# Performance work log

Measured on AMD Instinct MI355X. Metric: run time of the kernel, lower is better.

## Reference

```python
import jax, jax.numpy as jnp
import numpy as np

B, XD, PD, D, H = 512, 32768, 512, 64, 128  # batch, x_dim, proj_dim, latent_dim, per_dim_hidden
G1 = 1024  # gene projector hidden (hardcoded in module)


def _init(k, shape, fan_in):
    s = 1.0 / np.sqrt(fan_in)
    return jax.random.uniform(k, shape, jnp.float32, -s, s)


def setup_inputs() -> dict:
    key = jax.random.key(0)
    ks = jax.random.split(key, 16)
    return {
        "x": jax.random.normal(ks[0], (B, XD), jnp.float32),
        "z": jax.random.normal(ks[1], (B, D), jnp.float32),
        "perm": jax.random.permutation(ks[2], B).astype(jnp.int32),
        # shared gene projector
        "Wg1": _init(ks[3], (XD, G1), XD), "bg1": _init(ks[4], (G1,), XD),
        "Wg2": _init(ks[5], (G1, PD), G1), "bg2": _init(ks[6], (PD,), G1),
        # per-dimension 3-layer MLPs, stacked over D. Layer-1 weight [PD+1, H]
        # is split into the h-part Wh and the z-part Wz (last input column).
        "Wh": _init(ks[7], (D, PD, H), PD + 1),
        "Wz": _init(ks[8], (D, H), PD + 1),
        "b1": _init(ks[9], (D, H), PD + 1),
        "W2": _init(ks[10], (D, H, H), H), "b2": _init(ks[11], (D, H), H),
        "W3": _init(ks[12], (D, H), H), "b3": _init(ks[13], (D,), H),
    }


def reference(x, z, perm, Wg1, bg1, Wg2, bg2, Wh, Wz, b1, W2, b2, W3, b3):
    elu = jax.nn.elu
    # shared gene projector (eval mode: dropout = identity, no noise)
    h = elu(elu(x @ Wg1 + bg1) @ Wg2 + bg2)            # [B, PD]
    # batched layer-1 of all D per-dim nets; h-projection computed once and
    # reused for the marginal pass via permutation (h_shuffled = h[perm]).
    hWh = jnp.einsum('bp,dph->bdh', h, Wh)             # [B, D, H]
    zWz = z[:, :, None] * Wz[None]                     # [B, D, H]

    def head(a1_pre):
        a1 = elu(a1_pre)                               # [B, D, H]
        a2 = elu(jnp.einsum('bdh,dhk->bdk', a1, W2) + b2)
        return jnp.einsum('bdh,dh->bd', a2, W3) + b3   # [B, D] scalar scores

    joint_score = head(hWh + zWz + b1)                 # T(h, z_j)
    marg_score = head(hWh[perm] + zWz + b1)            # T(h_shuffled, z_j)

    emas = jnp.ones((D,), x.dtype)                     # buffer init = ones, eval: no update
    et = jnp.mean(jnp.exp(marg_score), axis=0)         # [D]
    mi = jnp.mean(joint_score, axis=0) - jnp.log(et / emas)
    return -jnp.mean(mi)
```

## Files before the change

### kernel.cpp

```cpp
#include <hip/hip_runtime.h>
#include <hip/hip_bf16.h>
#include <math.h>

#define B_  512
#define XD_ 32768
#define PD_ 512
#define D_  64
#define H_  128
#define G1_ 1024

typedef __attribute__((ext_vector_type(8))) short short8v;
typedef __attribute__((ext_vector_type(4))) float floatx4;

__device__ __forceinline__ float eluf(float v) { return v > 0.f ? v : expm1f(v); }

__device__ __forceinline__ void split8t(const float* c, short8v& h, short8v& l) {
    unsigned hu[8], lu[8];
    #pragma unroll
    for (int j = 0; j < 8; j++) {
        unsigned u = __float_as_uint(c[j]);
        hu[j] = u & 0xFFFF0000u;
        float res = c[j] - __uint_as_float(hu[j]);
        lu[j] = __float_as_uint(res);
    }
    uint4 hp, lp;
    hp.x = __builtin_amdgcn_perm(hu[1], hu[0], 0x07060302u);
    hp.y = __builtin_amdgcn_perm(hu[3], hu[2], 0x07060302u);
    hp.z = __builtin_amdgcn_perm(hu[5], hu[4], 0x07060302u);
    hp.w = __builtin_amdgcn_perm(hu[7], hu[6], 0x07060302u);
    lp.x = __builtin_amdgcn_perm(lu[1], lu[0], 0x07060302u);
    lp.y = __builtin_amdgcn_perm(lu[3], lu[2], 0x07060302u);
    lp.z = __builtin_amdgcn_perm(lu[5], lu[4], 0x07060302u);
    lp.w = __builtin_amdgcn_perm(lu[7], lu[6], 0x07060302u);
    h = __builtin_bit_cast(short8v, hp);
    l = __builtin_bit_cast(short8v, lp);
}

__global__ __launch_bounds__(256) void k_trs(const float* __restrict__ x,
                                             ushort* __restrict__ xh,
                                             ushort* __restrict__ xl) {
    const int k0 = blockIdx.x * 64;
    const int m0 = blockIdx.y * 64;
    const int t = threadIdx.x;
    const int m = t & 63;
    const int kq = t >> 6;
    #pragma unroll
    for (int i = 0; i < 2; i++) {
        int kg = kq * 2 + i;
        const float* p = x + (size_t)(m0 + m) * XD_ + k0 + kg * 8;
        float4 v0 = *(const float4*)p, v1 = *(const float4*)(p + 4);
        float c[8] = {v0.x, v0.y, v0.z, v0.w, v1.x, v1.y, v1.z, v1.w};
        short8v h, l; split8t(c, h, l);
        size_t off = ((size_t)((k0 >> 3) + kg) * B_ + m0 + m) * 8;
        *(short8v*)(xh + off) = h;
        *(short8v*)(xl + off) = l;
    }
}

__global__ __launch_bounds__(256, 2) void k_gemm1t(const ushort* __restrict__ xh,
                                                   const ushort* __restrict__ xl,
                                                   const float* __restrict__ Wg1,
                                                   float* __restrict__ part,
                                                   int KS) {
    __shared__ ushort Ah[2][4 * 128 * 8], Al[2][4 * 128 * 8];
    __shared__ ushort Bh[2][4 * 128 * 8], Bl[2][4 * 128 * 8];
    const int nt = blockIdx.x, mt = blockIdx.y, ks = blockIdx.z;
    const int t = threadIdx.x;
    const int w = t >> 6, lane = t & 63;
    const int q = lane >> 4, l15 = lane & 15;
    const int wr = w >> 1, wc = w & 1;
    const int q4 = t >> 6, pr = t & 63;
    const int k0 = ks * KS;

    const size_t aoff = (((size_t)(k0 >> 3) + q4) * B_ + mt * 128 + pr) * 8;
    const ushort* Agh = xh + aoff;
    const ushort* Agl = xl + aoff;
    const float*  Bg  = Wg1 + (size_t)(k0 + q4 * 8) * G1_ + nt * 128 + pr * 2;

    floatx4 acc[4][4];
    #pragma unroll
    for (int i = 0; i < 4; i++)
        #pragma unroll
        for (int j = 0; j < 4; j++) acc[i][j] = (floatx4){0.f, 0.f, 0.f, 0.f};

    uint4 pAh0, pAh1, pAl0, pAl1;
    float2 pb[8];

    auto loadT = [&](int kt) {
        size_t o = (size_t)kt * B_;
        pAh0 = *(const uint4*)(Agh + o);
        pAh1 = *(const uint4*)(Agh + o + 512);
        pAl0 = *(const uint4*)(Agl + o);
        pAl1 = *(const uint4*)(Agl + o + 512);
        const float* p = Bg + (size_t)kt * G1_;
        #pragma unroll
        for (int kk = 0; kk < 8; kk++) pb[kk] = *(const float2*)(p + (size_t)kk * G1_);
    };

    auto stage = [&](int buf) {
        float c0[8], c1[8];
        #pragma unroll
        for (int kk = 0; kk < 8; kk++) { c0[kk] = pb[kk].x; c1[kk] = pb[kk].y; }
        short8v bh0, bl0, bh1, bl1;
        split8t(c0, bh0, bl0); split8t(c1, bh1, bl1);
        int n0 = pr * 2;
        int i0 = (q4 * 128 + (n0 ^ q4)) * 8;
        int i1 = (q4 * 128 + ((n0 + 1) ^ q4)) * 8;
        *(short8v*)&Bh[buf][i0] = bh0; *(short8v*)&Bl[buf][i0] = bl0;
        *(short8v*)&Bh[buf][i1] = bh1; *(short8v*)&Bl[buf][i1] = bl1;
        int ia0 = (q4 * 128 + (pr ^ q4)) * 8;
        *(uint4*)&Ah[buf][ia0] = pAh0;
        *(uint4*)&Al[buf][ia0] = pAl0;
        *(uint4*)&Ah[buf][ia0 + 512] = pAh1;
        *(uint4*)&Al[buf][ia0 + 512] = pAl1;
    };

    auto mma = [&](int buf) {
        short8v af[4], alf[4], bf[4], blf[4];
        #pragma unroll
        for (int i = 0; i < 4; i++) {
            int m = wr * 64 + i * 16 + l15;
            int idx = (q * 128 + (m ^ q)) * 8;
            af[i]  = *(const short8v*)&Ah[buf][idx];
            alf[i] = *(const short8v*)&Al[buf][idx];
        }
        #pragma unroll
        for (int j = 0; j < 4; j++) {
            int n = wc * 64 + j * 16 + l15;
            int idx = (q * 128 + (n ^ q)) * 8;
            bf[j]  = *(const short8v*)&Bh[buf][idx];
            blf[j] = *(const short8v*)&Bl[buf][idx];
        }
        #pragma unroll
        for (int i = 0; i < 4; i++)
            #pragma unroll
            for (int j = 0; j < 4; j++) {
                acc[i][j] = __builtin_amdgcn_mfma_f32_16x16x32_bf16(af[i],  bf[j],  acc[i][j], 0, 0, 0);
                acc[i][j] = __builtin_amdgcn_mfma_f32_16x16x32_bf16(af[i],  blf[j], acc[i][j], 0, 0, 0);
                acc[i][j] = __builtin_amdgcn_mfma_f32_16x16x32_bf16(alf[i], bf[j],  acc[i][j], 0, 0, 0);
            }
    };

    loadT(0);
    stage(0);
    loadT(32);
    asm volatile("s_waitcnt lgkmcnt(0)" ::: "memory");
    __builtin_amdgcn_s_barrier();

    const int NT = KS >> 5;
    for (int it = 0; it < NT - 1; it++) {
        const int cur = it & 1;
        stage(cur ^ 1);
        if (it + 2 < NT) loadT((it + 2) * 32);
        mma(cur);
        asm volatile("s_waitcnt lgkmcnt(0)" ::: "memory");
        __builtin_amdgcn_s_barrier();
    }
    mma((NT - 1) & 1);

    float* P = part + (size_t)ks * (B_ * G1_) + (size_t)(mt * 128) * G1_ + nt * 128;
    #pragma unroll
    for (int i = 0; i < 4; i++)
        #pragma unroll
        for (int j = 0; j < 4; j++) {
            int col = wc * 64 + j * 16 + l15;
            #pragma unroll
            for (int r = 0; r < 4; r++) {
                int row = wr * 64 + i * 16 + q * 4 + r;
                P[(size_t)row * G1_ + col] = acc[i][j][r];
            }
        }
}

__global__ __launch_bounds__(256, 2) void k_gemm1m(const float* __restrict__ x,
                                                   const float* __restrict__ Wg1,
                                                   float* __restrict__ part,
                                                   int KS) {
    __shared__ ushort Ah[4 * 128 * 8], Al[4 * 128 * 8];
    __shared__ ushort Bh[4 * 128 * 8], Bl[4 * 128 * 8];
    const int nt = blockIdx.x, mt = blockIdx.y, ks = blockIdx.z;
    const int t = threadIdx.x;
    const int w = t >> 6, lane = t & 63;
    const int q = lane >> 4, l15 = lane & 15;
    const int wr = w >> 1, wc = w & 1;
    const int kbB = t >> 6, nb = t & 63;
    const int mA = t & 127, kbA = t >> 7;
    const int k0 = ks * KS;

    const float* Ag = x + (size_t)(mt * 128 + mA) * XD_ + k0 + kbA * 8;
    const float* Bg = Wg1 + (size_t)(k0 + kbB * 8) * G1_ + nt * 128 + nb * 2;

    floatx4 acc[4][4];
    #pragma unroll
    for (int i = 0; i < 4; i++)
        #pragma unroll
        for (int j = 0; j < 4; j++) acc[i][j] = (floatx4){0.f, 0.f, 0.f, 0.f};

    float4 pa0 = *(const float4*)(Ag);
    float4 pa1 = *(const float4*)(Ag + 4);
    float4 pa2 = *(const float4*)(Ag + 16);
    float4 pa3 = *(const float4*)(Ag + 20);
    float2 pb[8];
    #pragma unroll
    for (int kk = 0; kk < 8; kk++) pb[kk] = *(const float2*)(Bg + (size_t)kk * G1_);

    for (int kt = 0; kt < KS; kt += 32) {
        float cA0[8] = {pa0.x, pa0.y, pa0.z, pa0.w, pa1.x, pa1.y, pa1.z, pa1.w};
        float cA1[8] = {pa2.x, pa2.y, pa2.z, pa2.w, pa3.x, pa3.y, pa3.z, pa3.w};
        float c0[8], c1[8];
        #pragma unroll
        for (int kk = 0; kk < 8; kk++) { c0[kk] = pb[kk].x; c1[kk] = pb[kk].y; }
        short8v ah0, al0, ah1, al1, bh0, bl0, bh1, bl1;
        split8t(cA0, ah0, al0);
        split8t(cA1, ah1, al1);
        split8t(c0, bh0, bl0);
        split8t(c1, bh1, bl1);
        if (kt + 32 < KS) {
            pa0 = *(const float4*)(Ag + kt + 32);
            pa1 = *(const float4*)(Ag + kt + 36);
            pa2 = *(const float4*)(Ag + kt + 48);
            pa3 = *(const float4*)(Ag + kt + 52);
            const float* p = Bg + (size_t)(kt + 32) * G1_;
            #pragma unroll
            for (int kk = 0; kk < 8; kk++) pb[kk] = *(const float2*)(p + (size_t)kk * G1_);
        }
        {
            int ia0 = (kbA * 128 + (mA ^ kbA)) * 8;
            int ia1 = ((kbA + 2) * 128 + (mA ^ (kbA + 2))) * 8;
            *(short8v*)&Ah[ia0] = ah0; *(short8v*)&Al[ia0] = al0;
            *(short8v*)&Ah[ia1] = ah1; *(short8v*)&Al[ia1] = al1;
            int n0i = nb * 2;
            int i0 = (kbB * 128 + (n0i ^ kbB)) * 8;
            int i1 = (kbB * 128 + ((n0i + 1) ^ kbB)) * 8;
            *(short8v*)&Bh[i0] = bh0; *(short8v*)&Bl[i0] = bl0;
            *(short8v*)&Bh[i1] = bh1; *(short8v*)&Bl[i1] = bl1;
        }
        __syncthreads();
        short8v af[4], alf[4], bf[4], blf[4];
        #pragma unroll
        for (int i = 0; i < 4; i++) {
            int m = wr * 64 + i * 16 + l15;
            int idx = (q * 128 + (m ^ q)) * 8;
            af[i]  = *(const short8v*)&Ah[idx];
            alf[i] = *(const short8v*)&Al[idx];
        }
        #pragma unroll
        for (int j = 0; j < 4; j++) {
            int n = wc * 64 + j * 16 + l15;
            int idx = (q * 128 + (n ^ q)) * 8;
            bf[j]  = *(const short8v*)&Bh[idx];
            blf[j] = *(const short8v*)&Bl[idx];
        }
        #pragma unroll
        for (int i = 0; i < 4; i++)
            #pragma unroll
            for (int j = 0; j < 4; j++) {
                acc[i][j] = __builtin_amdgcn_mfma_f32_16x16x32_bf16(af[i],  bf[j],  acc[i][j], 0, 0, 0);
                acc[i][j] = __builtin_amdgcn_mfma_f32_16x16x32_bf16(af[i],  blf[j], acc[i][j], 0, 0, 0);
                acc[i][j] = __builtin_amdgcn_mfma_f32_16x16x32_bf16(alf[i], bf[j],  acc[i][j], 0, 0, 0);
            }
        __syncthreads();
    }
    float* P = part + (size_t)ks * (B_ * G1_) + (size_t)(mt * 128) * G1_ + nt * 128;
    #pragma unroll
    for (int i = 0; i < 4; i++)
        #pragma unroll
        for (int j = 0; j < 4; j++) {
            int col = wc * 64 + j * 16 + l15;
            #pragma unroll
            for (int r = 0; r < 4; r++) {
                int row = wr * 64 + i * 16 + q * 4 + r;
                P[(size_t)row * G1_ + col] = acc[i][j][r];
            }
        }
}

__global__ __launch_bounds__(256) void k_red1(const float* __restrict__ part,
                                              const float* __restrict__ bg1,
                                              ushort* __restrict__ Gh,
                                              ushort* __restrict__ Gl,
                                              int nparts) {
    int idx = (blockIdx.x * 256 + threadIdx.x) * 8;
    const int S = B_ * G1_;
    float c[8] = {};
    for (int k = 0; k < nparts; k++) {
        const float* p = part + (size_t)k * S + idx;
        float4 v0 = *(const float4*)p, v1 = *(const float4*)(p + 4);
        c[0] += v0.x; c[1] += v0.y; c[2] += v0.z; c[3] += v0.w;
        c[4] += v1.x; c[5] += v1.y; c[6] += v1.z; c[7] += v1.w;
    }
    int cb = idx & (G1_ - 1);
    float4 b0 = *(const float4*)(bg1 + cb), b1v = *(const float4*)(bg1 + cb + 4);
    c[0] = eluf(c[0] + b0.x); c[1] = eluf(c[1] + b0.y);
    c[2] = eluf(c[2] + b0.z); c[3] = eluf(c[3] + b0.w);
    c[4] = eluf(c[4] + b1v.x); c[5] = eluf(c[5] + b1v.y);
    c[6] = eluf(c[6] + b1v.z); c[7] = eluf(c[7] + b1v.w);
    short8v h, l; split8t(c, h, l);
    *(short8v*)(Gh + idx) = h;
    *(short8v*)(Gl + idx) = l;
}

__global__ __launch_bounds__(256, 2) void k_gemm2m(const ushort* __restrict__ Gh,
                                                   const ushort* __restrict__ Gl,
                                                   const float* __restrict__ Wg2,
                                                   float* __restrict__ part2) {
    __shared__ ushort Ah[4 * 64 * 8], Al[4 * 64 * 8];
    __shared__ ushort Bh[4 * 64 * 8], Bl[4 * 64 * 8];
    const int nt = blockIdx.x, mt = blockIdx.y, ks = blockIdx.z;
    const int t = threadIdx.x;
    const int w = t >> 6, lane = t & 63;
    const int q = lane >> 4, l15 = lane & 15;
    const int kb = (t >> 4) & 3;
    const int rb = (t & 15) | (w << 4);
    const int k0 = ks * 128;

    const int cB = t & 63, g = t >> 6;

    floatx4 acc[4];
    #pragma unroll
    for (int i = 0; i < 4; i++) acc[i] = (floatx4){0.f, 0.f, 0.f, 0.f};

    for (int kt = 0; kt < 128; kt += 32) {
        {
            const ushort* pH = Gh + (size_t)(mt * 64 + rb) * G1_ + k0 + kt + kb * 8;
            const ushort* pL = Gl + (size_t)(mt * 64 + rb) * G1_ + k0 + kt + kb * 8;
            uint4 vh = *(const uint4*)pH;
            uint4 vl = *(const uint4*)pL;
            int idx = (kb * 64 + (rb ^ kb)) * 8;
            *(uint4*)&Ah[idx] = vh;
            *(uint4*)&Al[idx] = vl;
        }
        {
            float c[8];
            const float* p = Wg2 + (size_t)(k0 + kt + g * 8) * PD_ + nt * 64 + cB;
            #pragma unroll
            for (int kk = 0; kk < 8; kk++) c[kk] = p[(size_t)kk * PD_];
            short8v h, l; split8t(c, h, l);
            int idx = (g * 64 + (cB ^ g)) * 8;
            *(short8v*)&Bh[idx] = h;
            *(short8v*)&Bl[idx] = l;
        }
        __syncthreads();
        short8v af[4], alf[4], bf, blf;
        #pragma unroll
        for (int i = 0; i < 4; i++) {
            int m = i * 16 + l15;
            int idx = (q * 64 + (m ^ q)) * 8;
            af[i]  = *(const short8v*)&Ah[idx];
            alf[i] = *(const short8v*)&Al[idx];
        }
        {
            int n = w * 16 + l15;
            int idx = (q * 64 + (n ^ q)) * 8;
            bf  = *(const short8v*)&Bh[idx];
            blf = *(const short8v*)&Bl[idx];
        }
        #pragma unroll
        for (int i = 0; i < 4; i++) {
            acc[i] = __builtin_amdgcn_mfma_f32_16x16x32_bf16(af[i],  bf,  acc[i], 0, 0, 0);
            acc[i] = __builtin_amdgcn_mfma_f32_16x16x32_bf16(af[i],  blf, acc[i], 0, 0, 0);
            acc[i] = __builtin_amdgcn_mfma_f32_16x16x32_bf16(alf[i], bf,  acc[i], 0, 0, 0);
        }
        __syncthreads();
    }
    float* P = part2 + (size_t)ks * (B_ * PD_) + (size_t)(mt * 64) * PD_ + nt * 64;
    #pragma unroll
    for (int i = 0; i < 4; i++) {
        int col = w * 16 + l15;
        #pragma unroll
        for (int r = 0; r < 4; r++) {
            int row = i * 16 + q * 4 + r;
            P[(size_t)row * PD_ + col] = acc[i][r];
        }
    }
}

__global__ __launch_bounds__(256) void k_red2(const float* __restrict__ part2,
                                              const float* __restrict__ bg2,
                                              ushort* __restrict__ hh,
                                              ushort* __restrict__ hl) {
    int idx = (blockIdx.x * 256 + threadIdx.x) * 8;
    const int S = B_ * PD_;
    float c[8] = {};
    #pragma unroll
    for (int k = 0; k < 8; k++) {
        const float* p = part2 + (size_t)k * S + idx;
        float4 v0 = *(const float4*)p, v1 = *(const float4*)(p + 4);
        c[0] += v0.x; c[1] += v0.y; c[2] += v0.z; c[3] += v0.w;
        c[4] += v1.x; c[5] += v1.y; c[6] += v1.z; c[7] += v1.w;
    }
    int cb = idx & (PD_ - 1);
    float4 b0 = *(const float4*)(bg2 + cb), b1v = *(const float4*)(bg2 + cb + 4);
    c[0] = eluf(c[0] + b0.x); c[1] = eluf(c[1] + b0.y);
    c[2] = eluf(c[2] + b0.z); c[3] = eluf(c[3] + b0.w);
    c[4] = eluf(c[4] + b1v.x); c[5] = eluf(c[5] + b1v.y);
    c[6] = eluf(c[6] + b1v.z); c[7] = eluf(c[7] + b1v.w);
    short8v h, l; split8t(c, h, l);
    *(short8v*)(hh + idx) = h;
    *(short8v*)(hl + idx) = l;
}

__global__ __launch_bounds__(256, 2) void k_hwh_m(const ushort* __restrict__ hh,
                                                  const ushort* __restrict__ hl,
                                                  const float* __restrict__ Wh,
                                                  float* __restrict__ hWh) {
    __shared__ ushort Ah[4 * 64 * 8], Al[4 * 64 * 8];
    __shared__ ushort Bh[4 * 128 * 8], Bl[4 * 128 * 8];
    const int d = blockIdx.x, mt = blockIdx.y;
    const int t = threadIdx.x;
    const int w = t >> 6, lane = t & 63;
    const int q = lane >> 4, l15 = lane & 15;
    const int kb = (t >> 4) & 3;
    const int rb = (t & 15) | (w << 4);

    const ushort* AgH = hh + (size_t)(mt * 64 + rb) * PD_ + kb * 8;
    const ushort* AgL = hl + (size_t)(mt * 64 + rb) * PD_ + kb * 8;
    const float* Bg = Wh + (size_t)d * (PD_ * H_) + (size_t)(kb * 8) * H_ + rb * 2;

    floatx4 acc[4][2];
    #pragma unroll
    for (int i = 0; i < 4; i++)
        #pragma unroll
        for (int j = 0; j < 2; j++) acc[i][j] = (floatx4){0.f, 0.f, 0.f, 0.f};

    uint4 pah = *(const uint4*)(AgH);
    uint4 pal = *(const uint4*)(AgL);
    float2 pb[8];
    #pragma unroll
    for (int kk = 0; kk < 8; kk++) pb[kk] = *(const float2*)(Bg + (size_t)kk * H_);

    for (int kt = 0; kt < PD_; kt += 32) {
        float c0[8], c1[8];
        #pragma unroll
        for (int kk = 0; kk < 8; kk++) { c0[kk] = pb[kk].x; c1[kk] = pb[kk].y; }
        short8v bh0, bl0, bh1, bl1;
        split8t(c0, bh0, bl0);
        split8t(c1, bh1, bl1);
        uint4 ah = pah, al = pal;
        if (kt + 32 < PD_) {
            pah = *(const uint4*)(AgH + kt + 32);
            pal = *(const uint4*)(AgL + kt + 32);
            const float* p = Bg + (size_t)(kt + 32) * H_;
            #pragma unroll
            for (int kk = 0; kk < 8; kk++) pb[kk] = *(const float2*)(p + (size_t)kk * H_);
        }
        {
            int idx = (kb * 64 + (rb ^ kb)) * 8;
            *(uint4*)&Ah[idx] = ah;
            *(uint4*)&Al[idx] = al;
            int n0i = rb * 2;
            int i0 = (kb * 128 + (n0i ^ kb)) * 8;
            int i1 = (kb * 128 + ((n0i + 1) ^ kb)) * 8;
            *(short8v*)&Bh[i0] = bh0; *(short8v*)&Bl[i0] = bl0;
            *(short8v*)&Bh[i1] = bh1; *(short8v*)&Bl[i1] = bl1;
        }
        __syncthreads();
        short8v af[4], alf[4], bf[2], blf[2];
        #pragma unroll
        for (int i = 0; i < 4; i++) {
            int m = i * 16 + l15;
            int idx = (q * 64 + (m ^ q)) * 8;
            af[i]  = *(const short8v*)&Ah[idx];
            alf[i] = *(const short8v*)&Al[idx];
        }
        #pragma unroll
        for (int j = 0; j < 2; j++) {
            int n = w * 32 + j * 16 + l15;
            int idx = (q * 128 + (n ^ q)) * 8;
            bf[j]  = *(const short8v*)&Bh[idx];
            blf[j] = *(const short8v*)&Bl[idx];
        }
        #pragma unroll
        for (int i = 0; i < 4; i++)
            #pragma unroll
            for (int j = 0; j < 2; j++) {
                acc[i][j] = __builtin_amdgcn_mfma_f32_16x16x32_bf16(af[i],  bf[j],  acc[i][j], 0, 0, 0);
                acc[i][j] = __builtin_amdgcn_mfma_f32_16x16x32_bf16(af[i],  blf[j], acc[i][j], 0, 0, 0);
                acc[i][j] = __builtin_amdgcn_mfma_f32_16x16x32_bf16(alf[i], bf[j],  acc[i][j], 0, 0, 0);
            }
        __syncthreads();
    }
    #pragma unroll
    for (int i = 0; i < 4; i++)
        #pragma unroll
        for (int j = 0; j < 2; j++) {
            int col = w * 32 + j * 16 + l15;
            #pragma unroll
            for (int r = 0; r < 4; r++) {
                int row = i * 16 + q * 4 + r;
                int b = mt * 64 + row;
                hWh[(size_t)b * (D_ * H_) + d * H_ + col] = acc[i][j][r];
            }
        }
}

__global__ __launch_bounds__(256, 2) void k_heads(const float* __restrict__ hWh,
                                                  const float* __restrict__ z,
                                                  const int* __restrict__ perm,
                                                  const float* __restrict__ Wz,
                                                  const float* __restrict__ b1,
                                                  const float* __restrict__ W2,
                                                  const float* __restrict__ b2,
                                                  const float* __restrict__ W3,
                                                  const float* __restrict__ b3,
                                                  float* __restrict__ jpart,
                                                  float* __restrict__ epart) {
    const int chunk = blockIdx.x;
    const int d = blockIdx.y;
    const int pass = blockIdx.z;
    const int t = threadIdx.x;
    const int b0 = chunk * 64;
    __shared__ ushort A1h[16 * 64 * 8];
    __shared__ ushort A1l[16 * 64 * 8];
    __shared__ float  BS[4096];
    ushort* Bh = (ushort*)BS;
    ushort* Bl = Bh + 4096;
    float*  sred = BS;

    const int w = t >> 6, lane = t & 63;
    const int q = lane >> 4, l15 = lane & 15;
    const int kb = (t >> 4) & 3;
    const int rb = (t & 15) | (w << 4);

    const float* W2d = W2 + (size_t)d * H_ * H_;
    const float* Wzd = Wz + d * H_;
    const float* b1d = b1 + d * H_;
    const float* b2d = b2 + d * H_;
    const float* W3d = W3 + d * H_;

    {
        int i = t >> 2;
        int kt = t & 3;
        int h0 = kt * 32;
        int bb = b0 + i;
        int src = (pass == 0) ? bb : perm[bb];
        float zv = z[bb * D_ + d];
        const float* hrow = hWh + (size_t)src * (D_ * H_) + d * H_;
        #pragma unroll
        for (int kq = 0; kq < 4; kq++) {
            float c[8];
            int kbase = h0 + kq * 8;
            float4 v0 = *(const float4*)(hrow + kbase);
            float4 v1 = *(const float4*)(hrow + kbase + 4);
            float4 w0 = *(const float4*)(Wzd + kbase);
            float4 w1 = *(const float4*)(Wzd + kbase + 4);
            float4 x0 = *(const float4*)(b1d + kbase);
            float4 x1 = *(const float4*)(b1d + kbase + 4);
            c[0] = eluf(v0.x + zv * w0.x + x0.x);
            c[1] = eluf(v0.y + zv * w0.y + x0.y);
            c[2] = eluf(v0.z + zv * w0.z + x0.z);
            c[3] = eluf(v0.w + zv * w0.w + x0.w);
            c[4] = eluf(v1.x + zv * w1.x + x1.x);
            c[5] = eluf(v1.y + zv * w1.y + x1.y);
            c[6] = eluf(v1.z + zv * w1.z + x1.z);
            c[7] = eluf(v1.w + zv * w1.w + x1.w);
            short8v hv, lv; split8t(c, hv, lv);
            int idx = ((kt * 4 + kq) * 64 + (i ^ kq)) * 8;
            *(short8v*)&A1h[idx] = hv;
            *(short8v*)&A1l[idx] = lv;
        }
    }
    __syncthreads();
    floatx4 acc[4][2];
    #pragma unroll
    for (int i = 0; i < 4; i++)
        #pragma unroll
        for (int j = 0; j < 2; j++) acc[i][j] = (floatx4){0.f, 0.f, 0.f, 0.f};
    for (int kt2 = 0; kt2 < 4; kt2++) {
        {
            float c0[8], c1[8];
            const float* p = W2d + (size_t)(kt2 * 32 + kb * 8) * H_ + rb * 2;
            #pragma unroll
            for (int kk = 0; kk < 8; kk++) {
                float2 v = *(const float2*)(p + (size_t)kk * H_);
                c0[kk] = v.x; c1[kk] = v.y;
            }
            short8v h0v, l0v, h1v, l1v;
            split8t(c0, h0v, l0v);
            split8t(c1, h1v, l1v);
            int n0i = rb * 2;
            int i0 = (kb * 128 + (n0i ^ kb)) * 8;
            int i1 = (kb * 128 + ((n0i + 1) ^ kb)) * 8;
            *(short8v*)&Bh[i0] = h0v; *(short8v*)&Bl[i0] = l0v;
            *(short8v*)&Bh[i1] = h1v; *(short8v*)&Bl[i1] = l1v;
        }
        __syncthreads();
        short8v af[4], alf[4], bf[2], blf[2];
        #pragma unroll
        for (int i = 0; i < 4; i++) {
            int m = i * 16 + l15;
            int idx = ((kt2 * 4 + q) * 64 + (m ^ q)) * 8;
            af[i]  = *(const short8v*)&A1h[idx];
            alf[i] = *(const short8v*)&A1l[idx];
        }
        #pragma unroll
        for (int j = 0; j < 2; j++) {
            int n = w * 32 + j * 16 + l15;
            int idx = (q * 128 + (n ^ q)) * 8;
            bf[j]  = *(const short8v*)&Bh[idx];
            blf[j] = *(const short8v*)&Bl[idx];
        }
        #pragma unroll
        for (int i = 0; i < 4; i++)
            #pragma unroll
            for (int j = 0; j < 2; j++) {
                acc[i][j] = __builtin_amdgcn_mfma_f32_16x16x32_bf16(af[i],  bf[j],  acc[i][j], 0, 0, 0);
                acc[i][j] = __builtin_amdgcn_mfma_f32_16x16x32_bf16(af[i],  blf[j], acc[i][j], 0, 0, 0);
                acc[i][j] = __builtin_amdgcn_mfma_f32_16x16x32_bf16(alf[i], bf[j],  acc[i][j], 0, 0, 0);
            }
        __syncthreads();
    }
    #pragma unroll
    for (int i = 0; i < 4; i++) {
        #pragma unroll
        for (int r = 0; r < 4; r++) {
            int b = i * 16 + q * 4 + r;
            float s = 0.f;
            #pragma unroll
            for (int j = 0; j < 2; j++) {
                int col = w * 32 + j * 16 + l15;
                float a2v = eluf(acc[i][j][r] + b2d[col]);
                s = fmaf(a2v, W3d[col], s);
            }
            sred[b * 64 + w * 16 + l15] = s;
        }
    }
    __syncthreads();
    float val = 0.f;
    if (t < 64) {
        float s = b3[d];
        const float4* row = (const float4*)&sred[t * 64];
        #pragma unroll
        for (int c = 0; c < 16; c++) {
            float4 v = row[c];
            s += v.x + v.y + v.z + v.w;
        }
        val = (pass == 0) ? s : expf(s);
        #pragma unroll
        for (int off = 32; off > 0; off >>= 1)
            val += __shfl_down(val, off, 64);
    }
    if (t == 0) {
        if (pass == 0) jpart[d * 8 + chunk] = val;
        else           epart[d * 8 + chunk] = val;
    }
}

__global__ void k_final(const float* __restrict__ jpart,
                        const float* __restrict__ epart,
                        float* __restrict__ out) {
    int t = threadIdx.x;
    float mj = 0.f, me = 0.f;
    #pragma unroll
    for (int c = 0; c < 8; c++) { mj += jpart[t * 8 + c]; me += epart[t * 8 + c]; }
    mj *= (1.f / 512.f);
    me *= (1.f / 512.f);
    float mi = mj - logf(me);
    #pragma unroll
    for (int off = 32; off > 0; off >>= 1) mi += __shfl_down(mi, off, 64);
    if (t == 0) out[0] = -mi * (1.f / 64.f);
}

extern "C" void kernel_launch(void* const* d_in, const int* in_sizes, int n_in,
                              void* d_out, int out_size, void* d_ws, size_t ws_size,
                              hipStream_t stream) {
    const float* x   = (const float*)d_in[0];
    const float* z   = (const float*)d_in[1];
    const int*  perm = (const int*)d_in[2];
    const float* Wg1 = (const float*)d_in[3];
    const float* bg1 = (const float*)d_in[4];
    const float* Wg2 = (const float*)d_in[5];
    const float* bg2 = (const float*)d_in[6];
    const float* Wh  = (const float*)d_in[7];
    const float* Wz  = (const float*)d_in[8];
    const float* b1  = (const float*)d_in[9];
    const float* W2  = (const float*)d_in[10];
    const float* b2  = (const float*)d_in[11];
    const float* W3  = (const float*)d_in[12];
    const float* b3  = (const float*)d_in[13];
    float* out = (float*)d_out;

    char* base = (char*)d_ws;
    const size_t PART_SLICE = (size_t)B_ * G1_ * sizeof(float);

    const size_t NEW_NEED = 16 * PART_SLICE + 67108864ull + 2097152 + 1048576 + 4096;

    if (ws_size >= NEW_NEED) {
        float* part  = (float*)base;
        ushort* xh   = (ushort*)(base + 33554432);
        ushort* xl   = (ushort*)(base + 67108864);
        float* hWh   = (float*)base;
        float* part2 = (float*)(base + 16777216);
        ushort* Gh   = (ushort*)(base + 100663296);
        ushort* Gl   = Gh + 524288;
        ushort* hh   = (ushort*)(base + 102760448);
        ushort* hl   = hh + 262144;
        float* jpart = (float*)(base + 103809024);
        float* epart = jpart + 512;

        k_trs<<<dim3(512, 8), 256, 0, stream>>>(x, xh, xl);
        k_gemm1t<<<dim3(8, 4, 16), 256, 0, stream>>>(xh, xl, Wg1, part, XD_ / 16);
        k_red1<<<256, 256, 0, stream>>>(part, bg1, Gh, Gl, 16);
        k_gemm2m<<<dim3(8, 8, 8), 256, 0, stream>>>(Gh, Gl, Wg2, part2);
        k_red2<<<128, 256, 0, stream>>>(part2, bg2, hh, hl);
        k_hwh_m<<<dim3(64, 8), 256, 0, stream>>>(hh, hl, Wh, hWh);
        k_heads<<<dim3(8, 64, 2), 256, 0, stream>>>(hWh, z, perm, Wz, b1, W2, b2, W3, b3,
                                                    jpart, epart);
        k_final<<<1, 64, 0, stream>>>(jpart, epart, out);
    } else {
        int nks = (ws_size >= (size_t)32 * PART_SLICE + 3145728 + 4096) ? 32 : 16;
        const int KS = XD_ / nks;
        const size_t partBytes = (size_t)nks * PART_SLICE;

        float* part  = (float*)base;
        float* hWh   = (float*)base;
        float* part2 = (float*)(base + 16777216);
        ushort* Gh   = (ushort*)(base + partBytes);
        ushort* Gl   = Gh + 524288;
        ushort* hh   = (ushort*)(base + partBytes + 2097152);
        ushort* hl   = hh + 262144;
        float* jpart = (float*)(base + partBytes + 3145728);
        float* epart = jpart + 512;

        k_gemm1m<<<dim3(8, 4, nks), 256, 0, stream>>>(x, Wg1, part, KS);
        k_red1<<<256, 256, 0, stream>>>(part, bg1, Gh, Gl, nks);
        k_gemm2m<<<dim3(8, 8, 8), 256, 0, stream>>>(Gh, Gl, Wg2, part2);
        k_red2<<<128, 256, 0, stream>>>(part2, bg2, hh, hl);
        k_hwh_m<<<dim3(64, 8), 256, 0, stream>>>(hh, hl, Wh, hWh);
        k_heads<<<dim3(8, 64, 2), 256, 0, stream>>>(hWh, z, perm, Wz, b1, W2, b2, W3, b3,
                                                    jpart, epart);
        k_final<<<1, 64, 0, stream>>>(jpart, epart, out);
    }
}
```

Before: 427.8 us.

## Double-buffer hWh GEMM and merge joint/marginal head passes into one block

The per-dimension hWh GEMM now uses double-buffered LDS tiles and a load/stage/mma pipeline, so the next tile's global loads and bf16 splitting overlap the current MFMAs, with one barrier per step. The heads kernel runs both passes (joint and permuted) inside one block instead of a z-dimension of the grid. This halves the block count and lets the W2 loads hit cache on the second pass. The final row reduction is spread across all 256 threads via a small shared array. The costs are doubled LDS in the GEMM and less parallelism in the heads kernel.

Result: no change. 422.6 us (-1.2%).

```diff
diff --git a/kernel.cpp b/kernel.cpp
--- a/kernel.cpp
+++ b/kernel.cpp
@@ -108,11 +108,11 @@
         int i1 = (q4 * 128 + ((n0 + 1) ^ q4)) * 8;
         *(short8v*)&Bh[buf][i0] = bh0; *(short8v*)&Bl[buf][i0] = bl0;
         *(short8v*)&Bh[buf][i1] = bh1; *(short8v*)&Bl[buf][i1] = bl1;
-        int ia0 = (q4 * 128 + (pr ^ q4)) * 8;
-        *(uint4*)&Ah[buf][ia0] = pAh0;
-        *(uint4*)&Al[buf][ia0] = pAl0;
-        *(uint4*)&Ah[buf][ia0 + 512] = pAh1;
-        *(uint4*)&Al[buf][ia0 + 512] = pAl1;
+        int ia = (q4 * 128 + (pr ^ q4)) * 8;
+        *(uint4*)&Ah[buf][ia] = pAh0;
+        *(uint4*)&Al[buf][ia] = pAl0;
+        *(uint4*)&Ah[buf][ia + 512] = pAh1;
+        *(uint4*)&Al[buf][ia + 512] = pAl1;
     };
 
     auto mma = [&](int buf) {
@@ -400,22 +400,23 @@
     *(short8v*)(hl + idx) = l;
 }
 
-__global__ __launch_bounds__(256, 2) void k_hwh_m(const ushort* __restrict__ hh,
+__global__ __launch_bounds__(256, 2) void k_hwh_t(const ushort* __restrict__ hh,
                                                   const ushort* __restrict__ hl,
                                                   const float* __restrict__ Wh,
                                                   float* __restrict__ hWh) {
-    __shared__ ushort Ah[4 * 64 * 8], Al[4 * 64 * 8];
-    __shared__ ushort Bh[4 * 128 * 8], Bl[4 * 128 * 8];
+    __shared__ ushort Ah[2][4 * 64 * 8], Al[2][4 * 64 * 8];
+    __shared__ ushort Bh[2][4 * 128 * 8], Bl[2][4 * 128 * 8];
     const int d = blockIdx.x, mt = blockIdx.y;
     const int t = threadIdx.x;
     const int w = t >> 6, lane = t & 63;
     const int q = lane >> 4, l15 = lane & 15;
     const int kb = (t >> 4) & 3;
     const int rb = (t & 15) | (w << 4);
+    const int kgB = t >> 6, pr = t & 63;
 
     const ushort* AgH = hh + (size_t)(mt * 64 + rb) * PD_ + kb * 8;
     const ushort* AgL = hl + (size_t)(mt * 64 + rb) * PD_ + kb * 8;
-    const float* Bg = Wh + (size_t)d * (PD_ * H_) + (size_t)(kb * 8) * H_ + rb * 2;
+    const float* Bg = Wh + (size_t)d * (PD_ * H_) + (size_t)(kgB * 8) * H_ + pr * 2;
 
     floatx4 acc[4][2];
     #pragma unroll
@@ -423,52 +424,48 @@
         #pragma unroll
         for (int j = 0; j < 2; j++) acc[i][j] = (floatx4){0.f, 0.f, 0.f, 0.f};
 
-    uint4 pah = *(const uint4*)(AgH);
-    uint4 pal = *(const uint4*)(AgL);
+    uint4 pah, pal;
     float2 pb[8];
-    #pragma unroll
-    for (int kk = 0; kk < 8; kk++) pb[kk] = *(const float2*)(Bg + (size_t)kk * H_);
-
-    for (int kt = 0; kt < PD_; kt += 32) {
+
+    auto loadT = [&](int kt) {
+        pah = *(const uint4*)(AgH + kt);
+        pal = *(const uint4*)(AgL + kt);
+        const float* p = Bg + (size_t)kt * H_;
+        #pragma unroll
+        for (int kk = 0; kk < 8; kk++) pb[kk] = *(const float2*)(p + (size_t)kk * H_);
+    };
+
+    auto stage = [&](int buf) {
         float c0[8], c1[8];
         #pragma unroll
         for (int kk = 0; kk < 8; kk++) { c0[kk] = pb[kk].x; c1[kk] = pb[kk].y; }
         short8v bh0, bl0, bh1, bl1;
-        split8t(c0, bh0, bl0);
-        split8t(c1, bh1, bl1);
-        uint4 ah = pah, al = pal;
-        if (kt + 32 < PD_) {
-            pah = *(const uint4*)(AgH + kt + 32);
-            pal = *(const uint4*)(AgL + kt + 32);
-            const float* p = Bg + (size_t)(kt + 32) * H_;
-            #pragma unroll
-            for (int kk = 0; kk < 8; kk++) pb[kk] = *(const float2*)(p + (size_t)kk * H_);
-        }
-        {
-            int idx = (kb * 64 + (rb ^ kb)) * 8;
-            *(uint4*)&Ah[idx] = ah;
-            *(uint4*)&Al[idx] = al;
-            int n0i = rb * 2;
-            int i0 = (kb * 128 + (n0i ^ kb)) * 8;
-            int i1 = (kb * 128 + ((n0i + 1) ^ kb)) * 8;
-            *(short8v*)&Bh[i0] = bh0; *(short8v*)&Bl[i0] = bl0;
-            *(short8v*)&Bh[i1] = bh1; *(short8v*)&Bl[i1] = bl1;
-        }
-        __syncthreads();
+        split8t(c0, bh0, bl0); split8t(c1, bh1, bl1);
+        int n0 = pr * 2;
+        int i0 = (kgB * 128 + (n0 ^ kgB)) * 8;
+        int i1 = (kgB * 128 + ((n0 + 1) ^ kgB)) * 8;
+        *(short8v*)&Bh[buf][i0] = bh0; *(short8v*)&Bl[buf][i0] = bl0;
+        *(short8v*)&Bh[buf][i1] = bh1; *(short8v*)&Bl[buf][i1] = bl1;
+        int ia = (kb * 64 + (rb ^ kb)) * 8;
+        *(uint4*)&Ah[buf][ia] = pah;
+        *(uint4*)&Al[buf][ia] = pal;
+    };
+
+    auto mma = [&](int buf) {
         short8v af[4], alf[4], bf[2], blf[2];
         #pragma unroll
         for (int i = 0; i < 4; i++) {
             int m = i * 16 + l15;
             int idx = (q * 64 + (m ^ q)) * 8;
-            af[i]  = *(const short8v*)&Ah[idx];
-            alf[i] = *(const short8v*)&Al[idx];
+            af[i]  = *(const short8v*)&Ah[buf][idx];
+            alf[i] = *(const short8v*)&Al[buf][idx];
         }
         #pragma unroll
         for (int j = 0; j < 2; j++) {
             int n = w * 32 + j * 16 + l15;
             int idx = (q * 128 + (n ^ q)) * 8;
-            bf[j]  = *(const short8v*)&Bh[idx];
-            blf[j] = *(const short8v*)&Bl[idx];
+            bf[j]  = *(const short8v*)&Bh[buf][idx];
+            blf[j] = *(const short8v*)&Bl[buf][idx];
         }
         #pragma unroll
         for (int i = 0; i < 4; i++)
@@ -478,8 +475,25 @@
                 acc[i][j] = __builtin_amdgcn_mfma_f32_16x16x32_bf16(af[i],  blf[j], acc[i][j], 0, 0, 0);
                 acc[i][j] = __builtin_amdgcn_mfma_f32_16x16x32_bf16(alf[i], bf[j],  acc[i][j], 0, 0, 0);
             }
-        __syncthreads();
-    }
+    };
+
+    loadT(0);
+    stage(0);
+    loadT(32);
+    asm volatile("s_waitcnt lgkmcnt(0)" ::: "memory");
+    __builtin_amdgcn_s_barrier();
+
+    const int NT = PD_ >> 5;
+    for (int it = 0; it < NT - 1; it++) {
+        const int cur = it & 1;
+        stage(cur ^ 1);
+        if (it + 2 < NT) loadT((it + 2) * 32);
+        mma(cur);
+        asm volatile("s_waitcnt lgkmcnt(0)" ::: "memory");
+        __builtin_amdgcn_s_barrier();
+    }
+    mma((NT - 1) & 1);
+
     #pragma unroll
     for (int i = 0; i < 4; i++)
         #pragma unroll
@@ -507,12 +521,12 @@
                                                   float* __restrict__ epart) {
     const int chunk = blockIdx.x;
     const int d = blockIdx.y;
-    const int pass = blockIdx.z;
     const int t = threadIdx.x;
     const int b0 = chunk * 64;
     __shared__ ushort A1h[16 * 64 * 8];
     __shared__ ushort A1l[16 * 64 * 8];
     __shared__ float  BS[4096];
+    __shared__ float  sq[4][64];
     ushort* Bh = (ushort*)BS;
     ushort* Bl = Bh + 4096;
     float*  sred = BS;
@@ -528,121 +542,132 @@
     const float* b2d = b2 + d * H_;
     const float* W3d = W3 + d * H_;
 
-    {
-        int i = t >> 2;
-        int kt = t & 3;
-        int h0 = kt * 32;
-        int bb = b0 + i;
-        int src = (pass == 0) ? bb : perm[bb];
-        float zv = z[bb * D_ + d];
-        const float* hrow = hWh + (size_t)src * (D_ * H_) + d * H_;
-        #pragma unroll
-        for (int kq = 0; kq < 4; kq++) {
-            float c[8];
-            int kbase = h0 + kq * 8;
-            float4 v0 = *(const float4*)(hrow + kbase);
-            float4 v1 = *(const float4*)(hrow + kbase + 4);
-            float4 w0 = *(const float4*)(Wzd + kbase);
-            float4 w1 = *(const float4*)(Wzd + kbase + 4);
-            float4 x0 = *(const float4*)(b1d + kbase);
-            float4 x1 = *(const float4*)(b1d + kbase + 4);
-            c[0] = eluf(v0.x + zv * w0.x + x0.x);
-            c[1] = eluf(v0.y + zv * w0.y + x0.y);
-            c[2] = eluf(v0.z + zv * w0.z + x0.z);
-            c[3] = eluf(v0.w + zv * w0.w + x0.w);
-            c[4] = eluf(v1.x + zv * w1.x + x1.x);
-            c[5] = eluf(v1.y + zv * w1.y + x1.y);
-            c[6] = eluf(v1.z + zv * w1.z + x1.z);
-            c[7] = eluf(v1.w + zv * w1.w + x1.w);
-            short8v hv, lv; split8t(c, hv, lv);
-            int idx = ((kt * 4 + kq) * 64 + (i ^ kq)) * 8;
-            *(short8v*)&A1h[idx] = hv;
-            *(short8v*)&A1l[idx] = lv;
-        }
-    }
-    __syncthreads();
-    floatx4 acc[4][2];
-    #pragma unroll
-    for (int i = 0; i < 4; i++)
-        #pragma unroll
-        for (int j = 0; j < 2; j++) acc[i][j] = (floatx4){0.f, 0.f, 0.f, 0.f};
-    for (int kt2 = 0; kt2 < 4; kt2++) {
+    float result0 = 0.f, result1 = 0.f;
+    for (int pass = 0; pass < 2; pass++) {
         {
-            float c0[8], c1[8];
-            const float* p = W2d + (size_t)(kt2 * 32 + kb * 8) * H_ + rb * 2;
-            #pragma unroll
-            for (int kk = 0; kk < 8; kk++) {
-                float2 v = *(const float2*)(p + (size_t)kk * H_);
-                c0[kk] = v.x; c1[kk] = v.y;
-            }
-            short8v h0v, l0v, h1v, l1v;
-            split8t(c0, h0v, l0v);
-            split8t(c1, h1v, l1v);
-            int n0i = rb * 2;
-            int i0 = (kb * 128 + (n0i ^ kb)) * 8;
-            int i1 = (kb * 128 + ((n0i + 1) ^ kb)) * 8;
-            *(short8v*)&Bh[i0] = h0v; *(short8v*)&Bl[i0] = l0v;
-            *(short8v*)&Bh[i1] = h1v; *(short8v*)&Bl[i1] = l1v;
+            int i = t >> 2;
+            int kt = t & 3;
+            int h0 = kt * 32;
+            int bb = b0 + i;
+            int src = (pass == 0) ? bb : perm[bb];
+            float zv = z[bb * D_ + d];
+            const float* hrow = hWh + (size_t)src * (D_ * H_) + d * H_;
+            #pragma unroll
+            for (int kq = 0; kq < 4; kq++) {
+                float c[8];
+                int kbase = h0 + kq * 8;
+                float4 v0 = *(const float4*)(hrow + kbase);
+                float4 v1 = *(const float4*)(hrow + kbase + 4);
+                float4 w0 = *(const float4*)(Wzd + kbase);
+                float4 w1 = *(const float4*)(Wzd + kbase + 4);
+                float4 x0 = *(const float4*)(b1d + kbase);
+                float4 x1 = *(const float4*)(b1d + kbase + 4);
+                c[0] = eluf(v0.x + zv * w0.x + x0.x);
+                c[1] = eluf(v0.y + zv * w0.y + x0.y);
+                c[2] = eluf(v0.z + zv * w0.z + x0.z);
+                c[3] = eluf(v0.w + zv * w0.w + x0.w);
+                c[4] = eluf(v1.x + zv * w1.x + x1.x);
+                c[5] = eluf(v1.y + zv * w1.y + x1.y);
+                c[6] = eluf(v1.z + zv * w1.z + x1.z);
+                c[7] = eluf(v1.w + zv * w1.w + x1.w);
+                short8v hv, lv; split8t(c, hv, lv);
+                int idx = ((kt * 4 + kq) * 64 + (i ^ kq)) * 8;
+                *(short8v*)&A1h[idx] = hv;
+                *(short8v*)&A1l[idx] = lv;
+            }
         }
         __syncthreads();
-        short8v af[4], alf[4], bf[2], blf[2];
+        floatx4 acc[4][2];
+        #pragma unroll
+        for (int i = 0; i < 4; i++)
+            #pragma unroll
+            for (int j = 0; j < 2; j++) acc[i][j] = (floatx4){0.f, 0.f, 0.f, 0.f};
+        for (int kt2 = 0; kt2 < 4; kt2++) {
+            {
+                float c0[8], c1[8];
+                const float* p = W2d + (size_t)(kt2 * 32 + kb * 8) * H_ + rb * 2;
+                #pragma unroll
+                for (int kk = 0; kk < 8; kk++) {
+                    float2 v = *(const float2*)(p + (size_t)kk * H_);
+                    c0[kk] = v.x; c1[kk] = v.y;
+                }
+                short8v h0v, l0v, h1v, l1v;
+                split8t(c0, h0v, l0v);
+                split8t(c1, h1v, l1v);
+                int n0i = rb * 2;
+                int i0 = (kb * 128 + (n0i ^ kb)) * 8;
+                int i1 = (kb * 128 + ((n0i + 1) ^ kb)) * 8;
+                *(short8v*)&Bh[i0] = h0v; *(short8v*)&Bl[i0] = l0v;
+                *(short8v*)&Bh[i1] = h1v; *(short8v*)&Bl[i1] = l1v;
+            }
+            __syncthreads();
+            short8v af[4], alf[4], bf[2], blf[2];
+            #pragma unroll
+            for (int i = 0; i < 4; i++) {
+                int m = i * 16 + l15;
+                int idx = ((kt2 * 4 + q) * 64 + (m ^ q)) * 8;
+                af[i]  = *(const short8v*)&A1h[idx];
+                alf[i] = *(const short8v*)&A1l[idx];
+            }
+            #pragma unroll
+            for (int j = 0; j < 2; j++) {
+                int n = w * 32 + j * 16 + l15;
+                int idx = (q * 128 + (n ^ q)) * 8;
+                bf[j]  = *(const short8v*)&Bh[idx];
+                blf[j] = *(const short8v*)&Bl[idx];
+            }
+            #pragma unroll
+            for (int i = 0; i < 4; i++)
+                #pragma unroll
+                for (int j = 0; j < 2; j++) {
+                    acc[i][j] = __builtin_amdgcn_mfma_f32_16x16x32_bf16(af[i],  bf[j],  acc[i][j], 0, 0, 0);
+                    acc[i][j] = __builtin_amdgcn_mfma_f32_16x16x32_bf16(af[i],  blf[j], acc[i][j], 0, 0, 0);
+                    acc[i][j] = __builtin_amdgcn_mfma_f32_16x16x32_bf16(alf[i], bf[j],  acc[i][j], 0, 0, 0);
+                }
+            __syncthreads();
+        }
         #pragma unroll
         for (int i = 0; i < 4; i++) {
-            int m = i * 16 + l15;
-            int idx = ((kt2 * 4 + q) * 64 + (m ^ q)) * 8;
-            af[i]  = *(const short8v*)&A1h[idx];
-            alf[i] = *(const short8v*)&A1l[idx];
-        }
-        #pragma unroll
-        for (int j = 0; j < 2; j++) {
-            int n = w * 32 + j * 16 + l15;
-            int idx = (q * 128 + (n ^ q)) * 8;
-            bf[j]  = *(const short8v*)&Bh[idx];
-            blf[j] = *(const short8v*)&Bl[idx];
-        }
-        #pragma unroll
-        for (int i = 0; i < 4; i++)
-            #pragma unroll
-            for (int j = 0; j < 2; j++) {
-                acc[i][j] = __builtin_amdgcn_mfma_f32_16x16x32_bf16(af[i],  bf[j],  acc[i][j], 0, 0, 0);
-                acc[i][j] = __builtin_amdgcn_mfma_f32_16x16x32_bf16(af[i],  blf[j], acc[i][j], 0, 0, 0);
-                acc[i][j] = __builtin_amdgcn_mfma_f32_16x16x32_bf16(alf[i], bf[j],  acc[i][j], 0, 0, 0);
-            }
+            #pragma unroll
+            for (int r = 0; r < 4; r++) {
+                int b = i * 16 + q * 4 + r;
+                float s = 0.f;
+                #pragma unroll
+                for (int j = 0; j < 2; j++) {
+                    int col = w * 32 + j * 16 + l15;
+                    float a2v = eluf(acc[i][j][r] + b2d[col]);
+                    s = fmaf(a2v, W3d[col], s);
+                }
+                sred[b * 64 + w * 16 + l15] = s;
+            }
+        }
         __syncthreads();
-    }
-    #pragma unroll
-    for (int i = 0; i < 4; i++) {
-        #pragma unroll
-        for (int r = 0; r < 4; r++) {
-            int b = i * 16 + q * 4 + r;
-            float s = 0.f;
-            #pragma unroll
-            for (int j = 0; j < 2; j++) {
-                int col = w * 32 + j * 16 + l15;
-                float a2v = eluf(acc[i][j][r] + b2d[col]);
-                s = fmaf(a2v, W3d[col], s);
-            }
-            sred[b * 64 + w * 16 + l15] = s;
-        }
-    }
-    __syncthreads();
-    float val = 0.f;
-    if (t < 64) {
-        float s = b3[d];
-        const float4* row = (const float4*)&sred[t * 64];
-        #pragma unroll
-        for (int c = 0; c < 16; c++) {
-            float4 v = row[c];
-            s += v.x + v.y + v.z + v.w;
-        }
-        val = (pass == 0) ? s : expf(s);
-        #pragma unroll
-        for (int off = 32; off > 0; off >>= 1)
-            val += __shfl_down(val, off, 64);
+        {
+            int rrow = t & 63, qd = t >> 6;
+            const float4* rp = (const float4*)&sred[rrow * 64 + qd * 16];
+            float ps = 0.f;
+            #pragma unroll
+            for (int c = 0; c < 4; c++) {
+                float4 v = rp[c];
+                ps += v.x + v.y + v.z + v.w;
+            }
+            sq[qd][rrow] = ps;
+        }
+        __syncthreads();
+        float val = 0.f;
+        if (t < 64) {
+            float s = b3[d] + sq[0][t] + sq[1][t] + sq[2][t] + sq[3][t];
+            val = (pass == 0) ? s : expf(s);
+            #pragma unroll
+            for (int off = 32; off > 0; off >>= 1)
+                val += __shfl_down(val, off, 64);
+        }
+        if (t == 0) { if (pass == 0) result0 = val; else result1 = val; }
+        __syncthreads();
     }
     if (t == 0) {
-        if (pass == 0) jpart[d * 8 + chunk] = val;
-        else           epart[d * 8 + chunk] = val;
+        jpart[d * 8 + chunk] = result0;
+        epart[d * 8 + chunk] = result1;
     }
 }
 
@@ -703,9 +728,9 @@
         k_red1<<<256, 256, 0, stream>>>(part, bg1, Gh, Gl, 16);
         k_gemm2m<<<dim3(8, 8, 8), 256, 0, stream>>>(Gh, Gl, Wg2, part2);
         k_red2<<<128, 256, 0, stream>>>(part2, bg2, hh, hl);
-        k_hwh_m<<<dim3(64, 8), 256, 0, stream>>>(hh, hl, Wh, hWh);
-        k_heads<<<dim3(8, 64, 2), 256, 0, stream>>>(hWh, z, perm, Wz, b1, W2, b2, W3, b3,
-                                                    jpart, epart);
+        k_hwh_t<<<dim3(64, 8), 256, 0, stream>>>(hh, hl, Wh, hWh);
+        k_heads<<<dim3(8, 64), 256, 0, stream>>>(hWh, z, perm, Wz, b1, W2, b2, W3, b3,
+                                                 jpart, epart);
         k_final<<<1, 64, 0, stream>>>(jpart, epart, out);
     } else {
         int nks = (ws_size >= (size_t)32 * PART_SLICE + 3145728 + 4096) ? 32 : 16;
@@ -726,9 +751,9 @@
         k_red1<<<256, 256, 0, stream>>>(part, bg1, Gh, Gl, nks);
         k_gemm2m<<<dim3(8, 8, 8), 256, 0, stream>>>(Gh, Gl, Wg2, part2);
         k_red2<<<128, 256, 0, stream>>>(part2, bg2, hh, hl);
-        k_hwh_m<<<dim3(64, 8), 256, 0, stream>>>(hh, hl, Wh, hWh);
-        k_heads<<<dim3(8, 64, 2), 256, 0, stream>>>(hWh, z, perm, Wz, b1, W2, b2, W3, b3,
-                                                    jpart, epart);
+        k_hwh_t<<<dim3(64, 8), 256, 0, stream>>>(hh, hl, Wh, hWh);
+        k_heads<<<dim3(8, 64), 256, 0, stream>>>(hWh, z, perm, Wz, b1, W2, b2, W3, b3,
+                                                 jpart, epart);
         k_final<<<1, 64, 0, stream>>>(jpart, epart, out);
     }
 }
```
